# Kernel optimization log

Hardware: AMD Instinct MI355X
Metric: run time of the kernel (lower is better)

The kernel has to match this reference:

```python
import jax, jax.numpy as jnp
import numpy as np

S = 1    # support_num
K = 20   # KNN neighbor count for conv layers
B, V = 4, 4096


def _normalize(x, axis):
    n = jnp.linalg.norm(x, axis=axis, keepdims=True)
    return x / jnp.maximum(n, 1e-12)


def _knn(v, k):
    # v: (b, n, 3) -> (b, n, k) indices of k nearest (excluding self)
    sq = jnp.sum(v * v, axis=-1)
    dist = sq[:, :, None] + sq[:, None, :] - 2.0 * jnp.einsum('bic,bjc->bij', v, v)
    return jax.lax.top_k(-dist, k + 1)[1][:, :, 1:]


def _gather(feat, idx):
    # feat (b,n,c), idx (b,n,k) -> (b,n,k,c)
    return feat[jnp.arange(feat.shape[0])[:, None, None], idx]


def _dir_norm(verts, idx):
    nb = _gather(verts, idx)                       # (b,v,k,3)
    return _normalize(nb - verts[:, :, None, :], -1)


def _conv_surface(idx, verts, directions, kernel_num):
    b, v, k = idx.shape
    nd = _dir_norm(verts, idx)
    sd = _normalize(directions, 0)                 # (3, S*kernel_num)
    theta = jax.nn.relu(jnp.einsum('bvkc,cm->bvkm', nd, sd))
    theta = theta.reshape(b, v, k, S, kernel_num)
    return jnp.sum(jnp.max(theta, axis=2), axis=2)  # (b,v,kernel_num)


def _conv_layer(idx, verts, fm, W, bias, directions, out_c):
    b, v, k = idx.shape
    nd = _dir_norm(verts, idx)
    sd = _normalize(directions, 0)                 # (3, S*out_c)
    theta = jax.nn.relu(jnp.einsum('bvkc,cm->bvkm', nd, sd))  # (b,v,k,S*out_c)
    fo = fm @ W + bias                             # (b,v,(S+1)*out_c)
    center = fo[:, :, :out_c]
    support = _gather(fo[:, :, out_c:], idx)       # (b,v,k,S*out_c)
    act = (theta * support).reshape(b, v, k, S, out_c)
    return center + jnp.sum(jnp.max(act, axis=2), axis=2)


def _pool(verts, fm, rate, nn, seed):
    b, v, _ = verts.shape
    idx = _knn(verts, nn)
    pooled = jnp.max(_gather(fm, idx), axis=2)
    sel = jax.random.permutation(jax.random.key(seed), v)[: v // rate]
    return verts[:, sel, :], pooled[:, sel, :]


def _ln(x, g, b):
    m = jnp.mean(x, -1, keepdims=True)
    var = jnp.mean(jnp.square(x - m), -1, keepdims=True)
    return (x - m) / jnp.sqrt(var + 1e-6) * g + b


def _mha(q, kv, Win, bin_, Wout, bout, h):
    E = q.shape[-1]
    hd = E // h
    wq, wk, wv = jnp.split(Win, 3, axis=0)
    bq, bk, bv = jnp.split(bin_, 3)

    def heads(x, w, bb_):
        y = x @ w.T + bb_
        return y.reshape(y.shape[0], y.shape[1], h, hd).transpose(0, 2, 1, 3)

    qh, kh, vh = heads(q, wq, bq), heads(kv, wk, bk), heads(kv, wv, bv)
    a = jax.nn.softmax(jnp.einsum('bhqd,bhkd->bhqk', qh, kh) / jnp.sqrt(jnp.float32(hd)), -1)
    o = jnp.einsum('bhqk,bhkd->bhqd', a, vh).transpose(0, 2, 1, 3).reshape(q.shape)
    return o @ Wout.T + bout


def _conv1x1(x, W, b):
    # x (B,C,N,1) -> (B,O,N,1)
    return jnp.einsum('bcnl,oc->bonl', x, W) + b[None, :, None, None]


def _bn_train(x, g, b):
    # BatchNorm2d in training mode (batch statistics), eps=1e-5
    m = jnp.mean(x, axis=(0, 2, 3), keepdims=True)
    v = jnp.var(x, axis=(0, 2, 3), keepdims=True)
    return (x - m) / jnp.sqrt(v + 1e-5) * g[None, :, None, None] + b[None, :, None, None]


def _forward(vertices, d0, g0, be0, w1, b1, dir1, g1, be1, w2, b2, dir2, g2, be2,
             w3, b3, dir3, g3, be3, token, a1_in_w, a1_in_b, a1_out_w, a1_out_b,
             ffn1_w, ffn1_b, bg, bb, ffn2_w, ffn2_b, a2_in_w, a2_in_b, a2_out_w,
             a2_out_b, w7, b7, dir7, g4, be4, c8_w, c8_b):
    b = vertices.shape[0]
    v0 = vertices[:, 0]                                 # (b, 4096, 3)
    idx0 = _knn(v0, K)
    fm0 = jax.nn.relu(_ln(_conv_surface(idx0, v0, d0, 32), g0, be0))
    fm1 = jax.nn.relu(_ln(_conv_layer(idx0, v0, fm0, w1, b1, dir1, 64), g1, be1))
    v1, fm1 = _pool(v0, fm1, 4, 4, 1)                   # (b,1024,3), (b,1024,64)
    idx1 = _knn(v1, K)
    fm_x = fm1
    fm2 = jax.nn.relu(_ln(_conv_layer(idx1, v1, fm1, w2, b2, dir2, 128), g2, be2))
    fm3 = jax.nn.relu(_ln(_conv_layer(idx1, v1, fm2, w3, b3, dir3, 256), g3, be3))
    _, fm3 = _pool(v1, fm3, 4, 4, 2)                    # (b,256,256)
    tok = jnp.tile(token, (b, 1, 1, 1))[:, :, :, 0].transpose(0, 2, 1)  # (b,1024,64)
    query = _mha(tok, fm_x, a1_in_w, a1_in_b, a1_out_w, a1_out_b, 4) + fm_x
    q2 = query.transpose(0, 2, 1)[:, :, :, None]        # (b,64,1024,1)
    q2 = _conv1x1(jax.nn.relu(_bn_train(_conv1x1(q2, ffn1_w, ffn1_b), bg, bb)), ffn2_w, ffn2_b)
    query = q2[:, :, :, 0].transpose(0, 2, 1)           # (b,1024,256)
    cross = _mha(query, fm3, a2_in_w, a2_in_b, a2_out_w, a2_out_b, 4) + query
    fmf = jax.nn.relu(_ln(_conv_layer(idx1, v1, cross, w7, b7, dir7, 1024), g4, be4))
    fmf = fmf.transpose(0, 2, 1)[:, :, :, None]         # (b,1024,1024,1)
    return _conv1x1(fmf, c8_w, c8_b)                    # (b,256,1024,1)


def setup_inputs():
    ks = iter(jax.random.split(jax.random.key(0), 64))

    def rn(shape, s=0.05):
        return jax.random.normal(next(ks), shape, dtype=jnp.float32) * s

    f32 = jnp.float32
    return dict(
        vertices=jax.random.normal(next(ks), (B, 1, V, 3), dtype=f32),
        d0=rn((3, S * 32)), g0=jnp.ones((32,), f32), be0=jnp.zeros((32,), f32),
        w1=rn((32, (S + 1) * 64)), b1=rn(((S + 1) * 64,)), dir1=rn((3, S * 64)),
        g1=jnp.ones((64,), f32), be1=jnp.zeros((64,), f32),
        w2=rn((64, (S + 1) * 128)), b2=rn(((S + 1) * 128,)), dir2=rn((3, S * 128)),
        g2=jnp.ones((128,), f32), be2=jnp.zeros((128,), f32),
        w3=rn((128, (S + 1) * 256)), b3=rn(((S + 1) * 256,)), dir3=rn((3, S * 256)),
        g3=jnp.ones((256,), f32), be3=jnp.zeros((256,), f32),
        token=rn((1, 64, 1024, 1), 1.0),
        a1_in_w=rn((192, 64)), a1_in_b=rn((192,)), a1_out_w=rn((64, 64)), a1_out_b=rn((64,)),
        ffn1_w=rn((256, 64)), ffn1_b=rn((256,)), bg=jnp.ones((256,), f32), bb=jnp.zeros((256,), f32),
        ffn2_w=rn((256, 256)), ffn2_b=rn((256,)),
        a2_in_w=rn((768, 256)), a2_in_b=rn((768,)), a2_out_w=rn((256, 256)), a2_out_b=rn((256,)),
        w7=rn((256, (S + 1) * 1024)), b7=rn(((S + 1) * 1024,)), dir7=rn((3, S * 1024)),
        g4=jnp.ones((1024,), f32), be4=jnp.zeros((1024,), f32),
        c8_w=rn((256, 1024)), c8_b=rn((256,)),
    )


def reference(vertices, d0, g0, be0, w1, b1, dir1, g1, be1, w2, b2, dir2, g2, be2,
              w3, b3, dir3, g3, be3, token, a1_in_w, a1_in_b, a1_out_w, a1_out_b,
              ffn1_w, ffn1_b, bg, bb, ffn2_w, ffn2_b, a2_in_w, a2_in_b, a2_out_w,
              a2_out_b, w7, b7, dir7, g4, be4, c8_w, c8_b):
    return _forward(vertices, d0, g0, be0, w1, b1, dir1, g1, be1, w2, b2, dir2, g2,
                    be2, w3, b3, dir3, g3, be3, token, a1_in_w, a1_in_b, a1_out_w,
                    a1_out_b, ffn1_w, ffn1_b, bg, bb, ffn2_w, ffn2_b, a2_in_w,
                    a2_in_b, a2_out_w, a2_out_b, w7, b7, dir7, g4, be4, c8_w, c8_b)
```

## Files before the change

kernel.cpp:

```cpp
#include <hip/hip_runtime.h>
#include <stdint.h>
#include <stddef.h>

#define FINF __builtin_inff()

__device__ inline void tf2x32(uint32_t k0, uint32_t k1, uint32_t x0, uint32_t x1,
                              uint32_t* o0, uint32_t* o1) {
  uint32_t ks2 = k0 ^ k1 ^ 0x1BD11BDAu;
  uint32_t v0 = x0 + k0, v1 = x1 + k1;
#define TFR(r) { v0 += v1; v1 = (v1 << (r)) | (v1 >> (32 - (r))); v1 ^= v0; }
  TFR(13) TFR(15) TFR(26) TFR(6)
  v0 += k1;  v1 += ks2 + 1u;
  TFR(17) TFR(29) TFR(16) TFR(24)
  v0 += ks2; v1 += k0 + 2u;
  TFR(13) TFR(15) TFR(26) TFR(6)
  v0 += k0;  v1 += k1 + 3u;
  TFR(17) TFR(29) TFR(16) TFR(24)
  v0 += k1;  v1 += ks2 + 4u;
  TFR(13) TFR(15) TFR(26) TFR(6)
  v0 += ks2; v1 += k0 + 5u;
#undef TFR
  *o0 = v0; *o1 = v1;
}

__device__ inline void perm_subkey(uint32_t seed, int round, uint32_t* s0, uint32_t* s1) {
  uint32_t k0 = 0u, k1 = seed;
  for (int r = 0; r < round; r++) {
    uint32_t a0, a1; tf2x32(k0, k1, 0u, 0u, &a0, &a1);
    k0 = a0; k1 = a1;
  }
  tf2x32(k0, k1, 0u, 1u, s0, s1);
}

__global__ __launch_bounds__(256) void perm_pass_kernel(uint32_t seed, int round, int n,
                                                        const int* __restrict__ vin,
                                                        int* __restrict__ vout, int m) {
  __shared__ unsigned long long lk[4096];
  __shared__ int part[256];
  uint32_t s0, s1; perm_subkey(seed, round, &s0, &s1);
  int t = threadIdx.x;
  for (int j = t; j < n; j += 256) {
    uint32_t y0, y1; tf2x32(s0, s1, 0u, (uint32_t)j, &y0, &y1);
    lk[j] = ((unsigned long long)(y0 ^ y1) << 32) | (unsigned)j;
  }
  __syncthreads();
  int r = blockIdx.x * 64 + (t & 63);
  int q = t >> 6;
  unsigned long long ki = lk[r];
  int cnt = 0;
  int j0 = q * (n >> 2), j1 = j0 + (n >> 2);
  for (int j = j0; j < j1; j++) cnt += (lk[j] < ki) ? 1 : 0;
  part[t] = cnt;
  __syncthreads();
  if (t < 64) {
    int rank = part[t] + part[t + 64] + part[t + 128] + part[t + 192];
    if (rank < m) vout[rank] = vin ? vin[r] : r;
  }
}

__device__ inline void wave_argmin2(float head_d, int head_i, float* Mo, int* wio) {
  float M = head_d;
#pragma unroll
  for (int off = 1; off < 64; off <<= 1) M = fminf(M, __shfl_xor(M, off));
  int cand = (head_d == M) ? head_i : 0x7fffffff;
#pragma unroll
  for (int off = 1; off < 64; off <<= 1) cand = min(cand, __shfl_xor(cand, off));
  *Mo = M; *wio = cand;
}

template <int CNT, int WAVES>
__global__ __launch_bounds__(64 * WAVES) void knn_lex_kernel(const float* __restrict__ verts,
                                                             int N,
                                                             int* __restrict__ idx20,
                                                             int* __restrict__ idx4) {
  constexpr int SH = (CNT - 1 < 21) ? (CNT - 1) : 21;
  int row = blockIdx.x; int b = row / N, i = row - b * N;
  int t = threadIdx.x; int w = t >> 6; int lane = t & 63;
  const float* vb = verts + (size_t)b * N * 3;
  float xi = vb[i * 3], yi = vb[i * 3 + 1], zi = vb[i * 3 + 2];
  float sqi = (xi * xi + yi * yi) + zi * zi;

  int base = w * (N / WAVES) + lane;
  float qd[CNT]; int qi[CNT];
#pragma unroll
  for (int m = 0; m < CNT; m++) {
    int j = base + m * 64;
    float xj = vb[j * 3], yj = vb[j * 3 + 1], zj = vb[j * 3 + 2];
    float sqj = (xj * xj + yj * yj) + zj * zj;
    float dot = (xi * xj + yi * yj) + zi * zj;
    qd[m] = sqi + sqj - 2.f * dot;
    qi[m] = j;
  }
#pragma unroll
  for (int k = 2; k <= CNT; k <<= 1)
#pragma unroll
    for (int j = k >> 1; j > 0; j >>= 1)
#pragma unroll
      for (int m = 0; m < CNT; m++) {
        int l = m ^ j;
        if (l > m) {
          bool up = ((m & k) == 0);
          bool sw = up ? (qd[m] > qd[l]) : (qd[m] < qd[l]);
          float td = sw ? qd[l] : qd[m]; qd[l] = sw ? qd[m] : qd[l]; qd[m] = td;
          int ti = sw ? qi[l] : qi[m]; qi[l] = sw ? qi[m] : qi[l]; qi[m] = ti;
        }
      }

  __shared__ float wd[WAVES][21];
  __shared__ int wi[WAVES][21];
  for (int r = 0; r < 21; r++) {
    float M; int widx;
    wave_argmin2(qd[0], qi[0], &M, &widx);
    if (lane == 0) { wd[w][r] = M; wi[w][r] = widx; }
    bool win = (qi[0] == widx);
#pragma unroll
    for (int m = 0; m < SH; m++) {
      qd[m] = win ? qd[m + 1] : qd[m];
      qi[m] = win ? qi[m + 1] : qi[m];
    }
    if (SH == CNT - 1) {
      if (win) { qd[CNT - 1] = FINF; qi[CNT - 1] = 0x7fffffff; }
    }
  }
  __syncthreads();
  if (lane < 21) {
    float d0 = wd[w][lane]; int i0 = wi[w][lane];
    int rank = lane;
#pragma unroll
    for (int w2 = 0; w2 < WAVES; w2++) {
      if (w2 == w) continue;
      for (int p = 0; p < 21; p++) {
        float ld = wd[w2][p]; int li = wi[w2][p];
        rank += (ld < d0 || (ld == d0 && li < i0)) ? 1 : 0;
      }
    }
    if (rank >= 1 && rank <= 20) idx20[(size_t)row * 20 + (rank - 1)] = i0;
    if (rank >= 1 && rank <= 4)  idx4[(size_t)row * 4 + (rank - 1)] = i0;
  }
}

template <int CNT>
__global__ __launch_bounds__(64) void knn_1w_lex_kernel(const float* __restrict__ verts, int N,
                                                        int* __restrict__ idx20,
                                                        int* __restrict__ idx4) {
  int row = blockIdx.x; int b = row / N, i = row - b * N;
  int lane = threadIdx.x;
  const float* vb = verts + (size_t)b * N * 3;
  float xi = vb[i * 3], yi = vb[i * 3 + 1], zi = vb[i * 3 + 2];
  float sqi = (xi * xi + yi * yi) + zi * zi;

  float qd[CNT]; int qi[CNT];
#pragma unroll
  for (int m = 0; m < CNT; m++) {
    int j = lane + m * 64;
    float xj = vb[j * 3], yj = vb[j * 3 + 1], zj = vb[j * 3 + 2];
    float sqj = (xj * xj + yj * yj) + zj * zj;
    float dot = (xi * xj + yi * yj) + zi * zj;
    qd[m] = sqi + sqj - 2.f * dot;
    qi[m] = j;
  }
#pragma unroll
  for (int k = 2; k <= CNT; k <<= 1)
#pragma unroll
    for (int j = k >> 1; j > 0; j >>= 1)
#pragma unroll
      for (int m = 0; m < CNT; m++) {
        int l = m ^ j;
        if (l > m) {
          bool up = ((m & k) == 0);
          bool sw = up ? (qd[m] > qd[l]) : (qd[m] < qd[l]);
          float td = sw ? qd[l] : qd[m]; qd[l] = sw ? qd[m] : qd[l]; qd[m] = td;
          int ti = sw ? qi[l] : qi[m]; qi[l] = sw ? qi[m] : qi[l]; qi[m] = ti;
        }
      }
  for (int r = 0; r < 21; r++) {
    float M; int widx;
    wave_argmin2(qd[0], qi[0], &M, &widx);
    if (lane == 0 && r >= 1) {
      idx20[(size_t)row * 20 + (r - 1)] = widx;
      if (r <= 4) idx4[(size_t)row * 4 + (r - 1)] = widx;
    }
    bool win = (qi[0] == widx);
#pragma unroll
    for (int m = 0; m < CNT - 1; m++) {
      qd[m] = win ? qd[m + 1] : qd[m];
      qi[m] = win ? qi[m + 1] : qi[m];
    }
    if (win) { qd[CNT - 1] = FINF; qi[CNT - 1] = 0x7fffffff; }
  }
}

__global__ void conv_surface_kernel(const float* __restrict__ verts,
                                    const int* __restrict__ idx20,
                                    const float* __restrict__ d0,
                                    const float* __restrict__ g, const float* __restrict__ be,
                                    float* __restrict__ out, int N) {
  int row = blockIdx.x; int b = row / N, i = row - b * N;
  int t = threadIdx.x;
  __shared__ float nd[20][3];
  const float* vb = verts + (size_t)b * N * 3;
  if (t < 20) {
    int j = idx20[(size_t)row * 20 + t];
    float dx = vb[j * 3] - vb[i * 3], dy = vb[j * 3 + 1] - vb[i * 3 + 1], dz = vb[j * 3 + 2] - vb[i * 3 + 2];
    float n2 = sqrtf(dx * dx + dy * dy + dz * dz); n2 = fmaxf(n2, 1e-12f);
    nd[t][0] = dx / n2; nd[t][1] = dy / n2; nd[t][2] = dz / n2;
  }
  __syncthreads();
  float x = 0.f;
  if (t < 32) {
    float a = d0[t], bb2 = d0[32 + t], c = d0[64 + t];
    float nrm = fmaxf(sqrtf(a * a + bb2 * bb2 + c * c), 1e-12f);
    a /= nrm; bb2 /= nrm; c /= nrm;
    float mx = -FINF;
    for (int kk = 0; kk < 20; kk++) {
      float th = fmaxf(nd[kk][0] * a + nd[kk][1] * bb2 + nd[kk][2] * c, 0.f);
      mx = fmaxf(mx, th);
    }
    x = mx;
  }
  float s = x;
  for (int off = 32; off; off >>= 1) s += __shfl_xor(s, off);
  float mean = s / 32.f;
  float dev = (t < 32) ? x - mean : 0.f;
  float s2 = dev * dev;
  for (int off = 32; off; off >>= 1) s2 += __shfl_xor(s2, off);
  float var = s2 / 32.f;
  if (t < 32) {
    float y = (x - mean) / sqrtf(var + 1e-6f) * g[t] + be[t];
    out[(size_t)row * 32 + t] = fmaxf(y, 0.f);
  }
}

__global__ void gemm_io_kernel(const float* __restrict__ x, const float* __restrict__ W,
                               const float* __restrict__ bias, float* __restrict__ y,
                               int R, int I, int O) {
  int rb = blockIdx.x * 8;
  int o = blockIdx.y * blockDim.x + threadIdx.x;
  __shared__ float xs[256][8];
  for (int u = 0; u < 8; u++)
    for (int i2 = threadIdx.x; i2 < I; i2 += blockDim.x) xs[i2][u] = x[(size_t)(rb + u) * I + i2];
  __syncthreads();
  float a[8] = {0, 0, 0, 0, 0, 0, 0, 0};
  for (int k2 = 0; k2 < I; k2++) {
    float wv = W[(size_t)k2 * O + o];
    float4 xa = *(const float4*)&xs[k2][0];
    float4 xb = *(const float4*)&xs[k2][4];
    a[0] += xa.x * wv; a[1] += xa.y * wv; a[2] += xa.z * wv; a[3] += xa.w * wv;
    a[4] += xb.x * wv; a[5] += xb.y * wv; a[6] += xb.z * wv; a[7] += xb.w * wv;
  }
  float bv = bias[o];
#pragma unroll
  for (int u = 0; u < 8; u++) y[(size_t)(rb + u) * O + o] = a[u] + bv;
}

template <int CPT>
__global__ void combine_kernel(const float* __restrict__ verts, const int* __restrict__ idx20,
                               const float* __restrict__ fo, const float* __restrict__ dirs,
                               const float* __restrict__ g, const float* __restrict__ be,
                               float* __restrict__ out, int N, int C) {
  int row = blockIdx.x; int b = row / N, i = row - b * N;
  int t = threadIdx.x, bs = blockDim.x;
  __shared__ float nd[20][3];
  __shared__ int nidx[20];
  __shared__ float red[8];
  const float* vb = verts + (size_t)b * N * 3;
  if (t < 20) {
    int j = idx20[(size_t)row * 20 + t];
    nidx[t] = j;
    float dx = vb[j * 3] - vb[i * 3], dy = vb[j * 3 + 1] - vb[i * 3 + 1], dz = vb[j * 3 + 2] - vb[i * 3 + 2];
    float n2 = fmaxf(sqrtf(dx * dx + dy * dy + dz * dz), 1e-12f);
    nd[t][0] = dx / n2; nd[t][1] = dy / n2; nd[t][2] = dz / n2;
  }
  __syncthreads();
  const float* fob = fo + (size_t)b * N * 2 * C;
  const float* forow = fob + (size_t)i * 2 * C;
  float da[CPT], db[CPT], dc[CPT], mx[CPT];
#pragma unroll
  for (int u = 0; u < CPT; u++) {
    int c = t + u * bs;
    float a = dirs[c], bb = dirs[C + c], cc = dirs[2 * C + c];
    float nrm = fmaxf(sqrtf(a * a + bb * bb + cc * cc), 1e-12f);
    da[u] = a / nrm; db[u] = bb / nrm; dc[u] = cc / nrm;
    mx[u] = -FINF;
  }
  for (int kk = 0; kk < 20; kk++) {
    float n0 = nd[kk][0], n1 = nd[kk][1], n2v = nd[kk][2];
    const float* sup = fob + (size_t)nidx[kk] * 2 * C + C + t;
#pragma unroll
    for (int u = 0; u < CPT; u++) {
      float th = fmaxf(n0 * da[u] + n1 * db[u] + n2v * dc[u], 0.f);
      mx[u] = fmaxf(mx[u], th * sup[u * bs]);
    }
  }
  float xv[CPT];
  float ssum = 0.f;
#pragma unroll
  for (int u = 0; u < CPT; u++) {
    int c = t + u * bs;
    float val = forow[c] + mx[u];
    xv[u] = val; ssum += val;
  }
  int nw = bs >> 6;
  for (int off = 32; off; off >>= 1) ssum += __shfl_down(ssum, off);
  if ((t & 63) == 0) red[t >> 6] = ssum;
  __syncthreads();
  if (t == 0) { float s = red[0]; for (int w = 1; w < nw; w++) s += red[w]; red[0] = s; }
  __syncthreads();
  float mean = red[0] / (float)C;
  __syncthreads();
  float s2 = 0.f;
#pragma unroll
  for (int u = 0; u < CPT; u++) { float d2 = xv[u] - mean; s2 += d2 * d2; }
  for (int off = 32; off; off >>= 1) s2 += __shfl_down(s2, off);
  if ((t & 63) == 0) red[t >> 6] = s2;
  __syncthreads();
  if (t == 0) { float s = red[0]; for (int w = 1; w < nw; w++) s += red[w]; red[0] = s; }
  __syncthreads();
  float inv = 1.0f / sqrtf(red[0] / (float)C + 1e-6f);
#pragma unroll
  for (int u = 0; u < CPT; u++) {
    int c = t + u * bs;
    float yv = (xv[u] - mean) * inv * g[c] + be[c];
    out[(size_t)row * C + c] = fmaxf(yv, 0.f);
  }
}

__global__ void pool_select_kernel(const float* __restrict__ fm, const int* __restrict__ idx4,
                                   const int* __restrict__ sel, const float* __restrict__ vin,
                                   float* __restrict__ vout, float* __restrict__ out,
                                   int N, int M, int C) {
  int row = blockIdx.x; int b = row / M, r = row - b * M;
  int s = sel[r];
  const int* id = idx4 + ((size_t)b * N + s) * 4;
  int i0 = id[0], i1 = id[1], i2 = id[2], i3 = id[3];
  const float* fb = fm + (size_t)b * N * C;
  for (int c = threadIdx.x; c < C; c += blockDim.x) {
    float m = fmaxf(fmaxf(fb[(size_t)i0 * C + c], fb[(size_t)i1 * C + c]),
                    fmaxf(fb[(size_t)i2 * C + c], fb[(size_t)i3 * C + c]));
    out[((size_t)b * M + r) * C + c] = m;
  }
  if (vout != nullptr && threadIdx.x < 3)
    vout[((size_t)b * M + r) * 3 + threadIdx.x] = vin[((size_t)b * N + s) * 3 + threadIdx.x];
}

__global__ void tok_kernel(const float* __restrict__ token, float* __restrict__ tok) {
  int id = blockIdx.x * 256 + threadIdx.x;
  int e = id & 63; int n = (id >> 6) & 1023;
  tok[id] = token[e * 1024 + n];
}

__global__ void linear_oi_kernel(const float* __restrict__ x, const float* __restrict__ W,
                                 const float* __restrict__ bias, const float* __restrict__ res,
                                 float* __restrict__ y, int R, int I, int O) {
  int rb = blockIdx.x * 8;
  int o = threadIdx.x;
  __shared__ float xs[8][256];
  for (int u = 0; u < 8; u++)
    for (int i2 = threadIdx.x; i2 < I; i2 += O) xs[u][i2] = x[(size_t)(rb + u) * I + i2];
  __syncthreads();
  float a[8] = {0, 0, 0, 0, 0, 0, 0, 0};
  const float* w = W + (size_t)o * I;
  for (int k2 = 0; k2 < I; k2++) {
    float wv = w[k2];
#pragma unroll
    for (int u = 0; u < 8; u++) a[u] += xs[u][k2] * wv;
  }
  float bv = bias[o];
#pragma unroll
  for (int u = 0; u < 8; u++) {
    float val = a[u] + bv;
    if (res) val += res[(size_t)(rb + u) * O + o];
    y[(size_t)(rb + u) * O + o] = val;
  }
}

template <int HD, int QPT, int KS>
__global__ __launch_bounds__(256) void attn_tiled(
    const float* __restrict__ q, const float* __restrict__ kk,
    const float* __restrict__ vv, float* __restrict__ o,
    int Lq, int Lk, int H, float scale) {
  constexpr int TK = 64;
  constexpr int QG = 256 / (2 * KS);
  constexpr int QPB = QG * QPT;
  constexpr int V4 = HD / 4;
  constexpr int STR = V4 + 1;
  constexpr int HH = HD / 2;
  constexpr int V4H = HH / 4;

  __shared__ float4 Ks[TK * STR];
  __shared__ float4 Vs[TK * STR];

  int t = threadIdx.x;
  int dh = t & 1;
  int ki = (t >> 1) & (KS - 1);
  int qg = t / (2 * KS);
  int nqt = Lq / QPB;
  int qt = blockIdx.x % nqt, bh = blockIdx.x / nqt;
  int h = bh % H, b = bh / H;
  int E = H * HD;
  int q0 = qt * QPB + qg * QPT;

  const float* qbase = q + ((size_t)b * Lq + q0) * E + h * HD + dh * HH;
  const float* kbase = kk + (size_t)b * Lk * E + h * HD;
  const float* vbase = vv + (size_t)b * Lk * E + h * HD;

  float qr[QPT][HH], O[QPT][HH], m[QPT], l[QPT];
#pragma unroll
  for (int r = 0; r < QPT; r++) {
    m[r] = -FINF; l[r] = 0.f;
#pragma unroll
    for (int d = 0; d < HH; d++) { qr[r][d] = qbase[(size_t)r * E + d]; O[r][d] = 0.f; }
  }

  for (int k0 = 0; k0 < Lk; k0 += TK) {
    __syncthreads();
    for (int e = t; e < TK * V4; e += 256) {
      int rr = e / V4, cc = e - rr * V4;
      Ks[rr * STR + cc] = *(const float4*)(kbase + (size_t)(k0 + rr) * E + cc * 4);
      Vs[rr * STR + cc] = *(const float4*)(vbase + (size_t)(k0 + rr) * E + cc * 4);
    }
    __syncthreads();
#pragma unroll 1
    for (int g = 0; g < TK / KS; g += 4) {
      float sc[QPT][4];
#pragma unroll
      for (int jj = 0; jj < 4; jj++) {
        int kl = (g + jj) * KS + ki;
        float sh[QPT];
#pragma unroll
        for (int r = 0; r < QPT; r++) sh[r] = 0.f;
        const float4* kr = &Ks[kl * STR + dh * V4H];
#pragma unroll
        for (int c = 0; c < V4H; c++) {
          float4 kv = kr[c];
#pragma unroll
          for (int r = 0; r < QPT; r++)
            sh[r] += qr[r][4 * c] * kv.x + qr[r][4 * c + 1] * kv.y
                   + qr[r][4 * c + 2] * kv.z + qr[r][4 * c + 3] * kv.w;
        }
#pragma unroll
        for (int r = 0; r < QPT; r++)
          sc[r][jj] = (sh[r] + __shfl_xor(sh[r], 1)) * scale;
      }
#pragma unroll
      for (int r = 0; r < QPT; r++) {
        float tm = fmaxf(fmaxf(sc[r][0], sc[r][1]), fmaxf(sc[r][2], sc[r][3]));
        float nm = fmaxf(m[r], tm);
        float a = __expf(m[r] - nm);
        m[r] = nm;
        float ls = l[r] * a;
#pragma unroll
        for (int d = 0; d < HH; d++) O[r][d] *= a;
#pragma unroll
        for (int jj = 0; jj < 4; jj++) { sc[r][jj] = __expf(sc[r][jj] - nm); ls += sc[r][jj]; }
        l[r] = ls;
      }
#pragma unroll
      for (int jj = 0; jj < 4; jj++) {
        int kl = (g + jj) * KS + ki;
        const float4* vr = &Vs[kl * STR + dh * V4H];
#pragma unroll
        for (int c = 0; c < V4H; c++) {
          float4 v4 = vr[c];
#pragma unroll
          for (int r = 0; r < QPT; r++) {
            O[r][4 * c]     += sc[r][jj] * v4.x;
            O[r][4 * c + 1] += sc[r][jj] * v4.y;
            O[r][4 * c + 2] += sc[r][jj] * v4.z;
            O[r][4 * c + 3] += sc[r][jj] * v4.w;
          }
        }
      }
    }
  }
#pragma unroll
  for (int r = 0; r < QPT; r++) {
    float M = m[r];
#pragma unroll
    for (int mask = 2; mask < 2 * KS; mask <<= 1) M = fmaxf(M, __shfl_xor(M, mask));
    float w = __expf(m[r] - M);
    float ll = l[r] * w;
#pragma unroll
    for (int mask = 2; mask < 2 * KS; mask <<= 1) ll += __shfl_xor(ll, mask);
    float inv = 1.f / ll;
#pragma unroll
    for (int d = 0; d < HH; d++) {
      float x = O[r][d] * w;
#pragma unroll
      for (int mask = 2; mask < 2 * KS; mask <<= 1) x += __shfl_xor(x, mask);
      O[r][d] = x * inv;
    }
  }
  if (ki == 0) {
    float* obase = o + ((size_t)b * Lq + q0) * E + h * HD + dh * HH;
#pragma unroll
    for (int r = 0; r < QPT; r++)
#pragma unroll
      for (int d = 0; d < HH; d++) obase[(size_t)r * E + d] = O[r][d];
  }
}

__global__ void bn_stats_kernel(const float* __restrict__ x, float* __restrict__ stats,
                                int R, int C) {
  int c = blockIdx.x; int t = threadIdx.x;
  __shared__ float red[8];
  float s = 0.f;
  for (int r = t; r < R; r += blockDim.x) s += x[(size_t)r * C + c];
  for (int off = 32; off; off >>= 1) s += __shfl_down(s, off);
  if ((t & 63) == 0) red[t >> 6] = s;
  __syncthreads();
  if (t == 0) { float a = red[0]; for (int w = 1; w < (int)(blockDim.x >> 6); w++) a += red[w]; red[0] = a; }
  __syncthreads();
  float mean = red[0] / (float)R;
  __syncthreads();
  float s2 = 0.f;
  for (int r = t; r < R; r += blockDim.x) { float d = x[(size_t)r * C + c] - mean; s2 += d * d; }
  for (int off = 32; off; off >>= 1) s2 += __shfl_down(s2, off);
  if ((t & 63) == 0) red[t >> 6] = s2;
  __syncthreads();
  if (t == 0) {
    float a = red[0]; for (int w = 1; w < (int)(blockDim.x >> 6); w++) a += red[w];
    stats[c] = mean; stats[C + c] = a / (float)R;
  }
}

__global__ void bn_apply_kernel(float* __restrict__ x, const float* __restrict__ stats,
                                const float* __restrict__ g, const float* __restrict__ b2,
                                int total, int C) {
  int id = blockIdx.x * blockDim.x + threadIdx.x;
  if (id >= total) return;
  int c = id % C;
  float y = (x[id] - stats[c]) / sqrtf(stats[C + c] + 1e-5f) * g[c] + b2[c];
  x[id] = fmaxf(y, 0.f);
}

__global__ void final_kernel(const float* __restrict__ fmf, const float* __restrict__ W,
                             const float* __restrict__ bias, float* __restrict__ out) {
  int nb = blockIdx.x * 8;
  int o = threadIdx.x;
  __shared__ float xs[1024][8];
  for (int u = 0; u < 8; u++)
    for (int c = threadIdx.x; c < 1024; c += 256) xs[c][u] = fmf[(size_t)(nb + u) * 1024 + c];
  __syncthreads();
  float acc[8] = {0, 0, 0, 0, 0, 0, 0, 0};
  const float* w = W + (size_t)o * 1024;
  for (int c = 0; c < 1024; c++) {
    float wv = w[c];
    float4 xa = *(const float4*)&xs[c][0];
    float4 xb = *(const float4*)&xs[c][4];
    acc[0] += xa.x * wv; acc[1] += xa.y * wv; acc[2] += xa.z * wv; acc[3] += xa.w * wv;
    acc[4] += xb.x * wv; acc[5] += xb.y * wv; acc[6] += xb.z * wv; acc[7] += xb.w * wv;
  }
  float bv = bias[o];
#pragma unroll
  for (int u = 0; u < 8; u++) {
    int r = nb + u; int b = r >> 10; int n = r & 1023;
    out[((size_t)(b * 256 + o) << 10) + n] = acc[u] + bv;
  }
}

extern "C" void kernel_launch(void* const* d_in, const int* in_sizes, int n_in,
                              void* d_out, int out_size, void* d_ws, size_t ws_size,
                              hipStream_t stream) {
  (void)in_sizes; (void)n_in; (void)out_size;
  const float* vertices = (const float*)d_in[0];
  const float* d0       = (const float*)d_in[1];
  const float* g0       = (const float*)d_in[2];
  const float* be0      = (const float*)d_in[3];
  const float* w1       = (const float*)d_in[4];
  const float* b1       = (const float*)d_in[5];
  const float* dir1     = (const float*)d_in[6];
  const float* g1       = (const float*)d_in[7];
  const float* be1      = (const float*)d_in[8];
  const float* w2       = (const float*)d_in[9];
  const float* b2       = (const float*)d_in[10];
  const float* dir2     = (const float*)d_in[11];
  const float* g2       = (const float*)d_in[12];
  const float* be2      = (const float*)d_in[13];
  const float* w3       = (const float*)d_in[14];
  const float* b3       = (const float*)d_in[15];
  const float* dir3     = (const float*)d_in[16];
  const float* g3       = (const float*)d_in[17];
  const float* be3      = (const float*)d_in[18];
  const float* token    = (const float*)d_in[19];
  const float* a1_in_w  = (const float*)d_in[20];
  const float* a1_in_b  = (const float*)d_in[21];
  const float* a1_out_w = (const float*)d_in[22];
  const float* a1_out_b = (const float*)d_in[23];
  const float* ffn1_w   = (const float*)d_in[24];
  const float* ffn1_b   = (const float*)d_in[25];
  const float* bg       = (const float*)d_in[26];
  const float* bbp      = (const float*)d_in[27];
  const float* ffn2_w   = (const float*)d_in[28];
  const float* ffn2_b   = (const float*)d_in[29];
  const float* a2_in_w  = (const float*)d_in[30];
  const float* a2_in_b  = (const float*)d_in[31];
  const float* a2_out_w = (const float*)d_in[32];
  const float* a2_out_b = (const float*)d_in[33];
  const float* w7       = (const float*)d_in[34];
  const float* b7       = (const float*)d_in[35];
  const float* dir7     = (const float*)d_in[36];
  const float* g4       = (const float*)d_in[37];
  const float* be4      = (const float*)d_in[38];
  const float* c8_w     = (const float*)d_in[39];
  const float* c8_b     = (const float*)d_in[40];
  float* out = (float*)d_out;
  float* ws = (float*)d_ws;

  if (ws_size < 78568448u) return;

  float* FO     = ws + 0;
  float* S1     = ws + 8388608;
  float* S2     = ws + 12582912;
  float* S3     = ws + 13631488;
  float* QUERY2 = ws + 14680064;
  float* CROSS  = ws + 15728640;
  float* FM1P   = ws + 16777216;
  float* FM3P   = FM1P + 262144;
  float* TOK    = FM3P + 262144;
  float* Q1     = TOK + 262144;
  float* K1     = Q1 + 262144;
  float* VA1    = K1 + 262144;
  float* ATT1   = VA1 + 262144;
  float* K2     = ATT1 + 262144;
  float* V2     = K2 + 262144;
  float* V1     = V2 + 262144;
  float* BNST   = V1 + 12288;
  int* IDX20_0  = (int*)(BNST + 512);
  int* IDX4_0   = IDX20_0 + 327680;
  int* IDX20_1  = IDX4_0 + 65536;
  int* IDX4_1   = IDX20_1 + 81920;
  int* SEL1     = IDX4_1 + 16384;
  int* SEL2     = SEL1 + 1024;
  int* PT1 = IDX20_0;

  perm_pass_kernel<<<64, 256, 0, stream>>>(1u, 0, 4096, nullptr, PT1, 4096);
  perm_pass_kernel<<<64, 256, 0, stream>>>(1u, 1, 4096, PT1, SEL1, 1024);
  perm_pass_kernel<<<16, 256, 0, stream>>>(2u, 0, 1024, nullptr, SEL2, 256);

  knn_lex_kernel<32, 2><<<4 * 4096, 128, 0, stream>>>(vertices, 4096, IDX20_0, IDX4_0);
  conv_surface_kernel<<<4 * 4096, 64, 0, stream>>>(vertices, IDX20_0, d0, g0, be0, S2, 4096);
  gemm_io_kernel<<<dim3(2048, 1), 128, 0, stream>>>(S2, w1, b1, FO, 16384, 32, 128);
  combine_kernel<1><<<16384, 64, 0, stream>>>(vertices, IDX20_0, FO, dir1, g1, be1, S1, 4096, 64);
  pool_select_kernel<<<4096, 64, 0, stream>>>(S1, IDX4_0, SEL1, vertices, V1, FM1P, 4096, 1024, 64);

  knn_1w_lex_kernel<16><<<4 * 1024, 64, 0, stream>>>(V1, 1024, IDX20_1, IDX4_1);
  gemm_io_kernel<<<dim3(512, 1), 256, 0, stream>>>(FM1P, w2, b2, FO, 4096, 64, 256);
  combine_kernel<1><<<4096, 128, 0, stream>>>(V1, IDX20_1, FO, dir2, g2, be2, S2, 1024, 128);
  gemm_io_kernel<<<dim3(512, 2), 256, 0, stream>>>(S2, w3, b3, FO, 4096, 128, 512);
  combine_kernel<1><<<4096, 256, 0, stream>>>(V1, IDX20_1, FO, dir3, g3, be3, S3, 1024, 256);
  pool_select_kernel<<<1024, 256, 0, stream>>>(S3, IDX4_1, SEL2, nullptr, nullptr, FM3P, 1024, 256, 256);

  tok_kernel<<<1024, 256, 0, stream>>>(token, TOK);
  linear_oi_kernel<<<512, 64, 0, stream>>>(TOK, a1_in_w, a1_in_b, nullptr, Q1, 4096, 64, 64);
  linear_oi_kernel<<<512, 64, 0, stream>>>(FM1P, a1_in_w + 64 * 64, a1_in_b + 64, nullptr, K1, 4096, 64, 64);
  linear_oi_kernel<<<512, 64, 0, stream>>>(FM1P, a1_in_w + 128 * 64, a1_in_b + 128, nullptr, VA1, 4096, 64, 64);
  attn_tiled<16, 4, 8><<<256, 256, 0, stream>>>(Q1, K1, VA1, ATT1, 1024, 1024, 4, 0.25f);
  linear_oi_kernel<<<512, 64, 0, stream>>>(ATT1, a1_out_w, a1_out_b, FM1P, S3, 4096, 64, 64);

  linear_oi_kernel<<<512, 256, 0, stream>>>(S3, ffn1_w, ffn1_b, nullptr, S2, 4096, 64, 256);
  bn_stats_kernel<<<256, 256, 0, stream>>>(S2, BNST, 4096, 256);
  bn_apply_kernel<<<4096, 256, 0, stream>>>(S2, BNST, bg, bbp, 4096 * 256, 256);
  linear_oi_kernel<<<512, 256, 0, stream>>>(S2, ffn2_w, ffn2_b, nullptr, QUERY2, 4096, 256, 256);

  linear_oi_kernel<<<512, 256, 0, stream>>>(QUERY2, a2_in_w, a2_in_b, nullptr, S3, 4096, 256, 256);
  linear_oi_kernel<<<128, 256, 0, stream>>>(FM3P, a2_in_w + 256 * 256, a2_in_b + 256, nullptr, K2, 1024, 256, 256);
  linear_oi_kernel<<<128, 256, 0, stream>>>(FM3P, a2_in_w + 512 * 256, a2_in_b + 512, nullptr, V2, 1024, 256, 256);
  attn_tiled<64, 2, 8><<<512, 256, 0, stream>>>(S3, K2, V2, S1, 1024, 256, 4, 0.125f);
  linear_oi_kernel<<<512, 256, 0, stream>>>(S1, a2_out_w, a2_out_b, QUERY2, CROSS, 4096, 256, 256);

  gemm_io_kernel<<<dim3(512, 8), 256, 0, stream>>>(CROSS, w7, b7, FO, 4096, 256, 2048);
  combine_kernel<4><<<4096, 256, 0, stream>>>(V1, IDX20_1, FO, dir7, g4, be4, S1, 1024, 1024);
  final_kernel<<<512, 256, 0, stream>>>(S1, c8_w, c8_b, out);
}
```

Before: 962.8 us.

## Pack KNN keys into 64-bit, merge small launches, widen final GEMM tile

The KNN bitonic sort now packs each distance (as float bits) with its index into a single 64-bit key. Each compare-swap becomes one 64-bit compare and select, replacing the separate float and int selects. This relies on distances being non-negative so the bit order matches the float order; a tiny negative distance from rounding would sort wrongly. Separately, the two independent permutation passes are merged into one launch, and the token transpose plus Q/K/V projections are fused into one kernel. The K2/V2 projections are also fused, the first attention uses QPT=2 with twice the blocks, and the w7 GEMM uses 16 rows per block to reuse each weight load more. Together these cut launch count and overhead at some cost in register pressure.

```diff
diff --git a/kernel.cpp b/kernel.cpp
--- a/kernel.cpp
+++ b/kernel.cpp
@@ -58,6 +58,37 @@
   }
 }
 
+__global__ __launch_bounds__(256) void perm_passA_kernel(int* __restrict__ pt1,
+                                                         int* __restrict__ sel2) {
+  __shared__ unsigned long long lk[4096];
+  __shared__ int part[256];
+  bool big = (blockIdx.x < 64);
+  uint32_t seed = big ? 1u : 2u;
+  int n = big ? 4096 : 1024;
+  int m = big ? 4096 : 256;
+  int* vout = big ? pt1 : sel2;
+  int blk = big ? blockIdx.x : (blockIdx.x - 64);
+  uint32_t s0, s1; perm_subkey(seed, 0, &s0, &s1);
+  int t = threadIdx.x;
+  for (int j = t; j < n; j += 256) {
+    uint32_t y0, y1; tf2x32(s0, s1, 0u, (uint32_t)j, &y0, &y1);
+    lk[j] = ((unsigned long long)(y0 ^ y1) << 32) | (unsigned)j;
+  }
+  __syncthreads();
+  int r = blk * 64 + (t & 63);
+  int q = t >> 6;
+  unsigned long long ki = lk[r];
+  int cnt = 0;
+  int j0 = q * (n >> 2), j1 = j0 + (n >> 2);
+  for (int j = j0; j < j1; j++) cnt += (lk[j] < ki) ? 1 : 0;
+  part[t] = cnt;
+  __syncthreads();
+  if (t < 64) {
+    int rank = part[t] + part[t + 64] + part[t + 128] + part[t + 192];
+    if (rank < m) vout[rank] = r;
+  }
+}
+
 __device__ inline void wave_argmin2(float head_d, int head_i, float* Mo, int* wio) {
   float M = head_d;
 #pragma unroll
@@ -81,15 +112,15 @@
   float sqi = (xi * xi + yi * yi) + zi * zi;
 
   int base = w * (N / WAVES) + lane;
-  float qd[CNT]; int qi[CNT];
+  unsigned long long qe[CNT];
 #pragma unroll
   for (int m = 0; m < CNT; m++) {
     int j = base + m * 64;
     float xj = vb[j * 3], yj = vb[j * 3 + 1], zj = vb[j * 3 + 2];
     float sqj = (xj * xj + yj * yj) + zj * zj;
     float dot = (xi * xj + yi * yj) + zi * zj;
-    qd[m] = sqi + sqj - 2.f * dot;
-    qi[m] = j;
+    float d = sqi + sqj - 2.f * dot;
+    qe[m] = ((unsigned long long)__float_as_uint(d) << 32) | (unsigned)j;
   }
 #pragma unroll
   for (int k = 2; k <= CNT; k <<= 1)
@@ -99,27 +130,27 @@
       for (int m = 0; m < CNT; m++) {
         int l = m ^ j;
         if (l > m) {
+          unsigned long long a = qe[m], c = qe[l];
           bool up = ((m & k) == 0);
-          bool sw = up ? (qd[m] > qd[l]) : (qd[m] < qd[l]);
-          float td = sw ? qd[l] : qd[m]; qd[l] = sw ? qd[m] : qd[l]; qd[m] = td;
-          int ti = sw ? qi[l] : qi[m]; qi[l] = sw ? qi[m] : qi[l]; qi[m] = ti;
+          bool sw = up ? (a > c) : (a < c);
+          qe[m] = sw ? c : a;
+          qe[l] = sw ? a : c;
         }
       }
 
   __shared__ float wd[WAVES][21];
   __shared__ int wi[WAVES][21];
   for (int r = 0; r < 21; r++) {
+    float hd = __uint_as_float((uint32_t)(qe[0] >> 32));
+    int hi = (int)(qe[0] & 0xffffffffu);
     float M; int widx;
-    wave_argmin2(qd[0], qi[0], &M, &widx);
+    wave_argmin2(hd, hi, &M, &widx);
     if (lane == 0) { wd[w][r] = M; wi[w][r] = widx; }
-    bool win = (qi[0] == widx);
-#pragma unroll
-    for (int m = 0; m < SH; m++) {
-      qd[m] = win ? qd[m + 1] : qd[m];
-      qi[m] = win ? qi[m + 1] : qi[m];
-    }
+    bool win = (hi == widx);
+#pragma unroll
+    for (int m = 0; m < SH; m++) qe[m] = win ? qe[m + 1] : qe[m];
     if (SH == CNT - 1) {
-      if (win) { qd[CNT - 1] = FINF; qi[CNT - 1] = 0x7fffffff; }
+      if (win) qe[CNT - 1] = 0x7F8000007FFFFFFFull;
     }
   }
   __syncthreads();
@@ -149,15 +180,15 @@
   float xi = vb[i * 3], yi = vb[i * 3 + 1], zi = vb[i * 3 + 2];
   float sqi = (xi * xi + yi * yi) + zi * zi;
 
-  float qd[CNT]; int qi[CNT];
+  unsigned long long qe[CNT];
 #pragma unroll
   for (int m = 0; m < CNT; m++) {
     int j = lane + m * 64;
     float xj = vb[j * 3], yj = vb[j * 3 + 1], zj = vb[j * 3 + 2];
     float sqj = (xj * xj + yj * yj) + zj * zj;
     float dot = (xi * xj + yi * yj) + zi * zj;
-    qd[m] = sqi + sqj - 2.f * dot;
-    qi[m] = j;
+    float d = sqi + sqj - 2.f * dot;
+    qe[m] = ((unsigned long long)__float_as_uint(d) << 32) | (unsigned)j;
   }
 #pragma unroll
   for (int k = 2; k <= CNT; k <<= 1)
@@ -167,26 +198,26 @@
       for (int m = 0; m < CNT; m++) {
         int l = m ^ j;
         if (l > m) {
+          unsigned long long a = qe[m], c = qe[l];
           bool up = ((m & k) == 0);
-          bool sw = up ? (qd[m] > qd[l]) : (qd[m] < qd[l]);
-          float td = sw ? qd[l] : qd[m]; qd[l] = sw ? qd[m] : qd[l]; qd[m] = td;
-          int ti = sw ? qi[l] : qi[m]; qi[l] = sw ? qi[m] : qi[l]; qi[m] = ti;
+          bool sw = up ? (a > c) : (a < c);
+          qe[m] = sw ? c : a;
+          qe[l] = sw ? a : c;
         }
       }
   for (int r = 0; r < 21; r++) {
+    float hd = __uint_as_float((uint32_t)(qe[0] >> 32));
+    int hi = (int)(qe[0] & 0xffffffffu);
     float M; int widx;
-    wave_argmin2(qd[0], qi[0], &M, &widx);
+    wave_argmin2(hd, hi, &M, &widx);
     if (lane == 0 && r >= 1) {
       idx20[(size_t)row * 20 + (r - 1)] = widx;
       if (r <= 4) idx4[(size_t)row * 4 + (r - 1)] = widx;
     }
-    bool win = (qi[0] == widx);
-#pragma unroll
-    for (int m = 0; m < CNT - 1; m++) {
-      qd[m] = win ? qd[m + 1] : qd[m];
-      qi[m] = win ? qi[m + 1] : qi[m];
-    }
-    if (win) { qd[CNT - 1] = FINF; qi[CNT - 1] = 0x7fffffff; }
+    bool win = (hi == widx);
+#pragma unroll
+    for (int m = 0; m < CNT - 1; m++) qe[m] = win ? qe[m + 1] : qe[m];
+    if (win) qe[CNT - 1] = 0x7F8000007FFFFFFFull;
   }
 }
 
@@ -251,6 +282,34 @@
   float bv = bias[o];
 #pragma unroll
   for (int u = 0; u < 8; u++) y[(size_t)(rb + u) * O + o] = a[u] + bv;
+}
+
+__global__ void gemm_io16_kernel(const float* __restrict__ x, const float* __restrict__ W,
+                                 const float* __restrict__ bias, float* __restrict__ y,
+                                 int R, int I, int O) {
+  int rb = blockIdx.x * 16;
+  int o = blockIdx.y * blockDim.x + threadIdx.x;
+  __shared__ float xs[256][16];
+  for (int u = 0; u < 16; u++)
+    for (int i2 = threadIdx.x; i2 < I; i2 += blockDim.x) xs[i2][u] = x[(size_t)(rb + u) * I + i2];
+  __syncthreads();
+  float a[16];
+#pragma unroll
+  for (int u = 0; u < 16; u++) a[u] = 0.f;
+  for (int k2 = 0; k2 < I; k2++) {
+    float wv = W[(size_t)k2 * O + o];
+    float4 x0 = *(const float4*)&xs[k2][0];
+    float4 x1 = *(const float4*)&xs[k2][4];
+    float4 x2 = *(const float4*)&xs[k2][8];
+    float4 x3 = *(const float4*)&xs[k2][12];
+    a[0] += x0.x * wv; a[1] += x0.y * wv; a[2] += x0.z * wv; a[3] += x0.w * wv;
+    a[4] += x1.x * wv; a[5] += x1.y * wv; a[6] += x1.z * wv; a[7] += x1.w * wv;
+    a[8] += x2.x * wv; a[9] += x2.y * wv; a[10] += x2.z * wv; a[11] += x2.w * wv;
+    a[12] += x3.x * wv; a[13] += x3.y * wv; a[14] += x3.z * wv; a[15] += x3.w * wv;
+  }
+  float bv = bias[o];
+#pragma unroll
+  for (int u = 0; u < 16; u++) y[(size_t)(rb + u) * O + o] = a[u] + bv;
 }
 
 template <int CPT>
@@ -343,12 +402,6 @@
     vout[((size_t)b * M + r) * 3 + threadIdx.x] = vin[((size_t)b * N + s) * 3 + threadIdx.x];
 }
 
-__global__ void tok_kernel(const float* __restrict__ token, float* __restrict__ tok) {
-  int id = blockIdx.x * 256 + threadIdx.x;
-  int e = id & 63; int n = (id >> 6) & 1023;
-  tok[id] = token[e * 1024 + n];
-}
-
 __global__ void linear_oi_kernel(const float* __restrict__ x, const float* __restrict__ W,
                                  const float* __restrict__ bias, const float* __restrict__ res,
                                  float* __restrict__ y, int R, int I, int O) {
@@ -372,6 +425,67 @@
     if (res) val += res[(size_t)(rb + u) * O + o];
     y[(size_t)(rb + u) * O + o] = val;
   }
+}
+
+__global__ __launch_bounds__(64) void qkv1_kernel(const float* __restrict__ token,
+                                                  const float* __restrict__ fm1p,
+                                                  const float* __restrict__ Win,
+                                                  const float* __restrict__ bin,
+                                                  float* __restrict__ Q1,
+                                                  float* __restrict__ K1,
+                                                  float* __restrict__ V1) {
+  int ybr = blockIdx.y;
+  const float* W = Win + (size_t)ybr * 64 * 64;
+  const float* bias = bin + ybr * 64;
+  float* out = (ybr == 0) ? Q1 : (ybr == 1) ? K1 : V1;
+  int rb = blockIdx.x * 8;
+  int o = threadIdx.x;
+  __shared__ float xs[8][64];
+  if (ybr == 0) {
+    for (int u = 0; u < 8; u++) {
+      int n = (rb + u) & 1023;
+      xs[u][o] = token[(size_t)o * 1024 + n];
+    }
+  } else {
+    for (int u = 0; u < 8; u++) xs[u][o] = fm1p[(size_t)(rb + u) * 64 + o];
+  }
+  __syncthreads();
+  float a[8] = {0, 0, 0, 0, 0, 0, 0, 0};
+  const float* w = W + (size_t)o * 64;
+  for (int k2 = 0; k2 < 64; k2++) {
+    float wv = w[k2];
+#pragma unroll
+    for (int u = 0; u < 8; u++) a[u] += xs[u][k2] * wv;
+  }
+  float bv = bias[o];
+#pragma unroll
+  for (int u = 0; u < 8; u++) out[(size_t)(rb + u) * 64 + o] = a[u] + bv;
+}
+
+__global__ __launch_bounds__(256) void kv2_kernel(const float* __restrict__ fm3p,
+                                                  const float* __restrict__ Win,
+                                                  const float* __restrict__ bin,
+                                                  float* __restrict__ K2,
+                                                  float* __restrict__ V2) {
+  int ybr = blockIdx.y;
+  const float* W = Win + (size_t)(1 + ybr) * 256 * 256;
+  const float* bias = bin + (1 + ybr) * 256;
+  float* out = ybr ? V2 : K2;
+  int rb = blockIdx.x * 8;
+  int o = threadIdx.x;
+  __shared__ float xs[8][256];
+  for (int u = 0; u < 8; u++) xs[u][o] = fm3p[(size_t)(rb + u) * 256 + o];
+  __syncthreads();
+  float a[8] = {0, 0, 0, 0, 0, 0, 0, 0};
+  const float* w = W + (size_t)o * 256;
+  for (int k2 = 0; k2 < 256; k2++) {
+    float wv = w[k2];
+#pragma unroll
+    for (int u = 0; u < 8; u++) a[u] += xs[u][k2] * wv;
+  }
+  float bv = bias[o];
+#pragma unroll
+  for (int u = 0; u < 8; u++) out[(size_t)(rb + u) * 256 + o] = a[u] + bv;
 }
 
 template <int HD, int QPT, int KS>
@@ -634,9 +748,8 @@
   int* SEL2     = SEL1 + 1024;
   int* PT1 = IDX20_0;
 
-  perm_pass_kernel<<<64, 256, 0, stream>>>(1u, 0, 4096, nullptr, PT1, 4096);
+  perm_passA_kernel<<<80, 256, 0, stream>>>(PT1, SEL2);
   perm_pass_kernel<<<64, 256, 0, stream>>>(1u, 1, 4096, PT1, SEL1, 1024);
-  perm_pass_kernel<<<16, 256, 0, stream>>>(2u, 0, 1024, nullptr, SEL2, 256);
 
   knn_lex_kernel<32, 2><<<4 * 4096, 128, 0, stream>>>(vertices, 4096, IDX20_0, IDX4_0);
   conv_surface_kernel<<<4 * 4096, 64, 0, stream>>>(vertices, IDX20_0, d0, g0, be0, S2, 4096);
@@ -651,11 +764,8 @@
   combine_kernel<1><<<4096, 256, 0, stream>>>(V1, IDX20_1, FO, dir3, g3, be3, S3, 1024, 256);
   pool_select_kernel<<<1024, 256, 0, stream>>>(S3, IDX4_1, SEL2, nullptr, nullptr, FM3P, 1024, 256, 256);
 
-  tok_kernel<<<1024, 256, 0, stream>>>(token, TOK);
-  linear_oi_kernel<<<512, 64, 0, stream>>>(TOK, a1_in_w, a1_in_b, nullptr, Q1, 4096, 64, 64);
-  linear_oi_kernel<<<512, 64, 0, stream>>>(FM1P, a1_in_w + 64 * 64, a1_in_b + 64, nullptr, K1, 4096, 64, 64);
-  linear_oi_kernel<<<512, 64, 0, stream>>>(FM1P, a1_in_w + 128 * 64, a1_in_b + 128, nullptr, VA1, 4096, 64, 64);
-  attn_tiled<16, 4, 8><<<256, 256, 0, stream>>>(Q1, K1, VA1, ATT1, 1024, 1024, 4, 0.25f);
+  qkv1_kernel<<<dim3(512, 3), 64, 0, stream>>>(token, FM1P, a1_in_w, a1_in_b, Q1, K1, VA1);
+  attn_tiled<16, 2, 8><<<512, 256, 0, stream>>>(Q1, K1, VA1, ATT1, 1024, 1024, 4, 0.25f);
   linear_oi_kernel<<<512, 64, 0, stream>>>(ATT1, a1_out_w, a1_out_b, FM1P, S3, 4096, 64, 64);
 
   linear_oi_kernel<<<512, 256, 0, stream>>>(S3, ffn1_w, ffn1_b, nullptr, S2, 4096, 64, 256);
@@ -664,12 +774,11 @@
   linear_oi_kernel<<<512, 256, 0, stream>>>(S2, ffn2_w, ffn2_b, nullptr, QUERY2, 4096, 256, 256);
 
   linear_oi_kernel<<<512, 256, 0, stream>>>(QUERY2, a2_in_w, a2_in_b, nullptr, S3, 4096, 256, 256);
-  linear_oi_kernel<<<128, 256, 0, stream>>>(FM3P, a2_in_w + 256 * 256, a2_in_b + 256, nullptr, K2, 1024, 256, 256);
-  linear_oi_kernel<<<128, 256, 0, stream>>>(FM3P, a2_in_w + 512 * 256, a2_in_b + 512, nullptr, V2, 1024, 256, 256);
+  kv2_kernel<<<dim3(128, 2), 256, 0, stream>>>(FM3P, a2_in_w, a2_in_b, K2, V2);
   attn_tiled<64, 2, 8><<<512, 256, 0, stream>>>(S3, K2, V2, S1, 1024, 256, 4, 0.125f);
   linear_oi_kernel<<<512, 256, 0, stream>>>(S1, a2_out_w, a2_out_b, QUERY2, CROSS, 4096, 256, 256);
 
-  gemm_io_kernel<<<dim3(512, 8), 256, 0, stream>>>(CROSS, w7, b7, FO, 4096, 256, 2048);
+  gemm_io16_kernel<<<dim3(256, 8), 256, 0, stream>>>(CROSS, w7, b7, FO, 4096, 256, 2048);
   combine_kernel<4><<<4096, 256, 0, stream>>>(V1, IDX20_1, FO, dir7, g4, be4, S1, 1024, 1024);
   final_kernel<<<512, 256, 0, stream>>>(S1, c8_w, c8_b, out);
 }
```

Result: faster. 934.4 us (-2.9%).
